# Kernel tuning notes

Measured on AMD Instinct MI355X. Metric: run time of the kernel, lower is better.

## Reference

```python
import jax, jax.numpy as jnp
import numpy as np

HIDDEN_DIM = 32
EDGE_DIM = 16
EDGE_HIDDEN = 64
N_EDGES = 250000


def setup_inputs() -> dict:
    key = jax.random.key(0)
    k1, k2, k3, k4, k5 = jax.random.split(key, 5)
    h_v = jax.random.normal(k1, (N_EDGES, HIDDEN_DIM), dtype=jnp.float32)
    h_w = jax.random.normal(k2, (N_EDGES, HIDDEN_DIM), dtype=jnp.float32)
    edge_features = jax.random.normal(k3, (N_EDGES, EDGE_DIM), dtype=jnp.float32)
    # Edge-network MLP params: edge_dim -> edge_hidden -> hidden_dim^2
    W1 = jax.random.normal(k4, (EDGE_DIM, EDGE_HIDDEN), dtype=jnp.float32) * (1.0 / np.sqrt(EDGE_DIM))
    b1 = jnp.zeros((EDGE_HIDDEN,), dtype=jnp.float32)
    W2 = jax.random.normal(k5, (EDGE_HIDDEN, HIDDEN_DIM * HIDDEN_DIM), dtype=jnp.float32) * (1.0 / np.sqrt(EDGE_HIDDEN))
    b2 = jnp.zeros((HIDDEN_DIM * HIDDEN_DIM,), dtype=jnp.float32)
    return {"h_v": h_v, "h_w": h_w, "edge_features": edge_features,
            "W1": W1, "b1": b1, "W2": W2, "b2": b2}


def reference(h_v, h_w, edge_features, W1, b1, W2, b2):
    # 1. Edge MLP: (n_edges, edge_dim) -> (n_edges, d*d)
    hdn = jax.nn.relu(edge_features @ W1 + b1)          # (E, edge_hidden)
    A = (hdn @ W2 + b2)                                  # (E, d*d)
    # 2. Reshape to per-edge matrices (E, d, d)
    d = h_w.shape[-1]
    A = A.reshape(-1, d, d)
    # 3. Per-edge matrix-vector product: M = A(e_vw) @ h_w
    messages = jnp.einsum('eij,ej->ei', A, h_w)          # (E, d)
    return messages
```

## Files before the change

### kernel.cpp

```cpp
#include <hip/hip_runtime.h>

typedef unsigned short u16;
typedef _Float16 f16x2 __attribute__((ext_vector_type(2)));
typedef _Float16 f16x8 __attribute__((ext_vector_type(8)));
typedef float    f32x4  __attribute__((ext_vector_type(4)));
typedef float    f32x16 __attribute__((ext_vector_type(16)));


union U4 { uint4 u; f16x8 h; u16 s[8]; };
union HU { f16x2 h2[4]; f16x8 h8; };

__global__ void prep_kernel(const float* __restrict__ W1,
                            const float* __restrict__ W2,
                            const float* __restrict__ b2,
                            u16* __restrict__ ws)
{
    int id = blockIdx.x * 256 + threadIdx.x;
    if (id < 8320) {
        int k2 = id >> 6, l = id & 63;
        int h = l >> 5, col = l & 31;
        U4 o;
        #pragma unroll
        for (int g = 0; g < 2; ++g) {
            int base4 = k2 * 16 + g * 8 + h * 4;
            f32x4 v;
            if (base4 < 2048) {
                int k1 = base4 >> 5, j32 = base4 & 31;
                v = *(const f32x4*)&W2[k1 * 1024 + col * 32 + j32];
            } else {
                v = *(const f32x4*)&b2[col * 32 + (base4 - 2048)];
            }
            #pragma unroll
            for (int j = 0; j < 4; ++j)
                o.h[g * 4 + j] = (_Float16)v[j];
        }
        *(uint4*)(ws + id * 8) = o.u;
    } else if (id < 8448) {
        int idx = id - 8320;
        int nt = idx >> 6, l = idx & 63;
        int h = l >> 5, col = nt * 32 + (l & 31);
        U4 o;
        #pragma unroll
        for (int g = 0; g < 2; ++g)
            #pragma unroll
            for (int j = 0; j < 4; ++j) {
                int k = g * 8 + h * 4 + j;
                o.h[g * 4 + j] = (_Float16)W1[k * 64 + col];
            }
        *(uint4*)(ws + id * 8) = o.u;
    }
}

#define STRIDE_T 98
#define SLICE_T  6400

__global__ __launch_bounds__(256, 3) void edge_kernel(
    const float* __restrict__ h_w,
    const float* __restrict__ ef,
    const float* __restrict__ b1,
    const u16*  __restrict__ ws,
    float* __restrict__ out,
    int E)
{
    __shared__ alignas(16) u16 ldsT[4 * SLICE_T];
    const int tid  = threadIdx.x;
    const int lane = tid & 63;
    const int wv   = tid >> 6;
    const int l31  = lane & 31;
    const int h    = lane >> 5;
    const int tileBase = (blockIdx.x * 4 + wv) * 96;
    if (tileBase >= E) return;
    u16* myT = ldsT + wv * SLICE_T;

    const uint4* Bf  = (const uint4*)ws;
    const uint4* W1f = (const uint4*)(ws + 8320 * 8);

    U4 w0, w1;
    w0.u = W1f[lane];
    w1.u = W1f[64 + lane];
    const float bb0 = b1[l31], bb1 = b1[32 + l31];
    #pragma unroll
    for (int mt = 0; mt < 3; ++mt) {
        int e = tileBase + mt * 32 + l31;
        bool ok = e < E;
        f32x4 g0 = {}, g1 = {};
        if (ok) {
            g0 = *(const f32x4*)&ef[e * 16 + h * 4];
            g1 = *(const f32x4*)&ef[e * 16 + 8 + h * 4];
        }
        U4 a;
        #pragma unroll
        for (int j = 0; j < 4; ++j) {
            a.h[j]     = (_Float16)g0[j];
            a.h[4 + j] = (_Float16)g1[j];
        }
        f32x16 c0 = {}, c1 = {};
        c0 = __builtin_amdgcn_mfma_f32_32x32x16_f16(a.h, w0.h, c0, 0, 0, 0);
        c1 = __builtin_amdgcn_mfma_f32_32x32x16_f16(a.h, w1.h, c1, 0, 0, 0);
        #pragma unroll
        for (int nt = 0; nt < 2; ++nt) {
            float bb = nt ? bb1 : bb0;
            int k1 = nt * 32 + l31;
            #pragma unroll
            for (int rp = 0; rp < 8; ++rp) {
                int r = 2 * rp;
                float v0 = fmaxf((nt ? c1[r]     : c0[r])     + bb, 0.f);
                float v1 = fmaxf((nt ? c1[r + 1] : c0[r + 1]) + bb, 0.f);
                f16x2 p = { (_Float16)v0, (_Float16)v1 };
                int e0 = mt * 32 + (r & 3) + 8 * (r >> 2) + 4 * h;
                *(unsigned int*)(myT + k1 * STRIDE_T + e0) =
                    __builtin_bit_cast(unsigned int, p);
            }
        }
    }
    if (lane < 48)
        *(unsigned int*)(myT + 64 * STRIDE_T + lane * 2) = 0x3C003C00u;

    f16x2 hwA[3][2][4];
    #pragma unroll
    for (int mt = 0; mt < 3; ++mt) {
        int e = tileBase + mt * 32 + l31;
        bool ok = e < E;
        f32x4 q0 = {}, q1 = {}, q2 = {}, q3 = {};
        if (ok) {
            const float* hp = h_w + (size_t)e * 32 + h * 4;
            q0 = *(const f32x4*)(hp);
            q1 = *(const f32x4*)(hp + 8);
            q2 = *(const f32x4*)(hp + 16);
            q3 = *(const f32x4*)(hp + 24);
        }
        hwA[mt][0][0] = f16x2{ (_Float16)q0[0], (_Float16)q0[1] };
        hwA[mt][0][1] = f16x2{ (_Float16)q0[2], (_Float16)q0[3] };
        hwA[mt][0][2] = f16x2{ (_Float16)q1[0], (_Float16)q1[1] };
        hwA[mt][0][3] = f16x2{ (_Float16)q1[2], (_Float16)q1[3] };
        hwA[mt][1][0] = f16x2{ (_Float16)q2[0], (_Float16)q2[1] };
        hwA[mt][1][1] = f16x2{ (_Float16)q2[2], (_Float16)q2[3] };
        hwA[mt][1][2] = f16x2{ (_Float16)q3[0], (_Float16)q3[1] };
        hwA[mt][1][3] = f16x2{ (_Float16)q3[2], (_Float16)q3[3] };
    }

    f32x16 acc0 = {}, acc1 = {}, acc2 = {};

    const uint4* bp = Bf + lane;
    #pragma unroll 2
    for (int k1 = 0; k1 < 65; ++k1) {
        U4 bf0, bf1;
        bf0.u = bp[(2 * k1) * 64];
        bf1.u = bp[(2 * k1 + 1) * 64];
        u16 t0 = myT[k1 * STRIDE_T + l31];
        u16 t1 = myT[k1 * STRIDE_T + 32 + l31];
        u16 t2 = myT[k1 * STRIDE_T + 64 + l31];
        #pragma unroll
        for (int mt = 0; mt < 3; ++mt) {
            union { u16 u; _Float16 f; } cv;
            cv.u = (mt == 0) ? t0 : (mt == 1) ? t1 : t2;
            f16x2 hh = { cv.f, cv.f };
            HU A;
            #pragma unroll
            for (int rr = 0; rr < 4; ++rr) A.h2[rr] = hh * hwA[mt][0][rr];
            if (mt == 0)      acc0 = __builtin_amdgcn_mfma_f32_32x32x16_f16(A.h8, bf0.h, acc0, 0, 0, 0);
            else if (mt == 1) acc1 = __builtin_amdgcn_mfma_f32_32x32x16_f16(A.h8, bf0.h, acc1, 0, 0, 0);
            else              acc2 = __builtin_amdgcn_mfma_f32_32x32x16_f16(A.h8, bf0.h, acc2, 0, 0, 0);
            #pragma unroll
            for (int rr = 0; rr < 4; ++rr) A.h2[rr] = hh * hwA[mt][1][rr];
            if (mt == 0)      acc0 = __builtin_amdgcn_mfma_f32_32x32x16_f16(A.h8, bf1.h, acc0, 0, 0, 0);
            else if (mt == 1) acc1 = __builtin_amdgcn_mfma_f32_32x32x16_f16(A.h8, bf1.h, acc1, 0, 0, 0);
            else              acc2 = __builtin_amdgcn_mfma_f32_32x32x16_f16(A.h8, bf1.h, acc2, 0, 0, 0);
        }
    }

    #pragma unroll
    for (int mt = 0; mt < 3; ++mt) {
        #pragma unroll
        for (int r = 0; r < 16; ++r) {
            int row = (r & 3) + 8 * (r >> 2) + 4 * h;
            int e = tileBase + mt * 32 + row;
            float v = (mt == 0) ? acc0[r] : (mt == 1) ? acc1[r] : acc2[r];
            if (e < E) out[(size_t)e * 32 + l31] = v;
        }
    }
}

extern "C" void kernel_launch(void* const* d_in, const int* in_sizes, int n_in,
                              void* d_out, int out_size, void* d_ws, size_t ws_size,
                              hipStream_t stream)
{
    const float* h_w = (const float*)d_in[1];
    const float* ef  = (const float*)d_in[2];
    const float* W1  = (const float*)d_in[3];
    const float* b1  = (const float*)d_in[4];
    const float* W2  = (const float*)d_in[5];
    const float* b2  = (const float*)d_in[6];
    float* out = (float*)d_out;
    const int E = in_sizes[1] / 32;
    u16* ws = (u16*)d_ws;

    prep_kernel<<<33, 256, 0, stream>>>(W1, W2, b2, ws);

    const int blocks = (E + 4 * 96 - 1) / (4 * 96);
    edge_kernel<<<blocks, 256, 0, stream>>>(h_w, ef, b1, ws, out, E);
}
```

Measured before the change: 49.19 us.

## Shrink per-wave tile to 64 edges and software-pipeline weight loads

Each wave now processes 64 edges instead of 96, which shrinks the LDS slice and the accumulator registers so the occupancy hint can rise from 3 to 4 blocks per CU. The global loads of the combined W2/b2 fragments are prefetched into a 4-deep register ring ahead of the MFMA loop, and the LDS hidden-activation values are loaded one iteration ahead. This is meant to hide global and LDS latency behind the matrix ops. In exchange, every wave re-reads the same weight stream for fewer edges, so total weight traffic per edge goes up.

```diff
diff --git a/kernel.cpp b/kernel.cpp
--- a/kernel.cpp
+++ b/kernel.cpp
@@ -51,10 +51,10 @@
     }
 }
 
-#define STRIDE_T 98
-#define SLICE_T  6400
-
-__global__ __launch_bounds__(256, 3) void edge_kernel(
+#define STRIDE_T 66
+#define SLICE_T  4352
+
+__global__ __launch_bounds__(256, 4) void edge_kernel(
     const float* __restrict__ h_w,
     const float* __restrict__ ef,
     const float* __restrict__ b1,
@@ -68,19 +68,27 @@
     const int wv   = tid >> 6;
     const int l31  = lane & 31;
     const int h    = lane >> 5;
-    const int tileBase = (blockIdx.x * 4 + wv) * 96;
+    const int tileBase = (blockIdx.x * 4 + wv) * 64;
     if (tileBase >= E) return;
     u16* myT = ldsT + wv * SLICE_T;
 
     const uint4* Bf  = (const uint4*)ws;
     const uint4* W1f = (const uint4*)(ws + 8320 * 8);
+    const uint4* bp  = Bf + lane;
+
+    U4 pipe[4][2];
+    #pragma unroll
+    for (int p = 0; p < 4; ++p) {
+        pipe[p][0].u = bp[(2 * p) * 64];
+        pipe[p][1].u = bp[(2 * p + 1) * 64];
+    }
 
     U4 w0, w1;
     w0.u = W1f[lane];
     w1.u = W1f[64 + lane];
     const float bb0 = b1[l31], bb1 = b1[32 + l31];
     #pragma unroll
-    for (int mt = 0; mt < 3; ++mt) {
+    for (int mt = 0; mt < 2; ++mt) {
         int e = tileBase + mt * 32 + l31;
         bool ok = e < E;
         f32x4 g0 = {}, g1 = {};
@@ -113,12 +121,12 @@
             }
         }
     }
-    if (lane < 48)
+    if (lane < 32)
         *(unsigned int*)(myT + 64 * STRIDE_T + lane * 2) = 0x3C003C00u;
 
-    f16x2 hwA[3][2][4];
-    #pragma unroll
-    for (int mt = 0; mt < 3; ++mt) {
+    f16x2 hwA[2][2][4];
+    #pragma unroll
+    for (int mt = 0; mt < 2; ++mt) {
         int e = tileBase + mt * 32 + l31;
         bool ok = e < E;
         f32x4 q0 = {}, q1 = {}, q2 = {}, q3 = {};
@@ -139,43 +147,48 @@
         hwA[mt][1][3] = f16x2{ (_Float16)q3[2], (_Float16)q3[3] };
     }
 
-    f32x16 acc0 = {}, acc1 = {}, acc2 = {};
-
-    const uint4* bp = Bf + lane;
-    #pragma unroll 2
+    f32x16 acc0 = {}, acc1 = {};
+
+    u16 t0 = myT[l31];
+    u16 t1 = myT[32 + l31];
+    #pragma unroll 4
     for (int k1 = 0; k1 < 65; ++k1) {
-        U4 bf0, bf1;
-        bf0.u = bp[(2 * k1) * 64];
-        bf1.u = bp[(2 * k1 + 1) * 64];
-        u16 t0 = myT[k1 * STRIDE_T + l31];
-        u16 t1 = myT[k1 * STRIDE_T + 32 + l31];
-        u16 t2 = myT[k1 * STRIDE_T + 64 + l31];
-        #pragma unroll
-        for (int mt = 0; mt < 3; ++mt) {
+        const int slot = k1 & 3;
+        const u16 c0v = t0, c1v = t1;
+        {
+            int kn = (k1 + 1 <= 64) ? k1 + 1 : 64;
+            t0 = myT[kn * STRIDE_T + l31];
+            t1 = myT[kn * STRIDE_T + 32 + l31];
+        }
+        #pragma unroll
+        for (int mt = 0; mt < 2; ++mt) {
             union { u16 u; _Float16 f; } cv;
-            cv.u = (mt == 0) ? t0 : (mt == 1) ? t1 : t2;
+            cv.u = (mt == 0) ? c0v : c1v;
             f16x2 hh = { cv.f, cv.f };
             HU A;
             #pragma unroll
             for (int rr = 0; rr < 4; ++rr) A.h2[rr] = hh * hwA[mt][0][rr];
-            if (mt == 0)      acc0 = __builtin_amdgcn_mfma_f32_32x32x16_f16(A.h8, bf0.h, acc0, 0, 0, 0);
-            else if (mt == 1) acc1 = __builtin_amdgcn_mfma_f32_32x32x16_f16(A.h8, bf0.h, acc1, 0, 0, 0);
-            else              acc2 = __builtin_amdgcn_mfma_f32_32x32x16_f16(A.h8, bf0.h, acc2, 0, 0, 0);
+            if (mt == 0) acc0 = __builtin_amdgcn_mfma_f32_32x32x16_f16(A.h8, pipe[slot][0].h, acc0, 0, 0, 0);
+            else         acc1 = __builtin_amdgcn_mfma_f32_32x32x16_f16(A.h8, pipe[slot][0].h, acc1, 0, 0, 0);
             #pragma unroll
             for (int rr = 0; rr < 4; ++rr) A.h2[rr] = hh * hwA[mt][1][rr];
-            if (mt == 0)      acc0 = __builtin_amdgcn_mfma_f32_32x32x16_f16(A.h8, bf1.h, acc0, 0, 0, 0);
-            else if (mt == 1) acc1 = __builtin_amdgcn_mfma_f32_32x32x16_f16(A.h8, bf1.h, acc1, 0, 0, 0);
-            else              acc2 = __builtin_amdgcn_mfma_f32_32x32x16_f16(A.h8, bf1.h, acc2, 0, 0, 0);
-        }
-    }
-
-    #pragma unroll
-    for (int mt = 0; mt < 3; ++mt) {
+            if (mt == 0) acc0 = __builtin_amdgcn_mfma_f32_32x32x16_f16(A.h8, pipe[slot][1].h, acc0, 0, 0, 0);
+            else         acc1 = __builtin_amdgcn_mfma_f32_32x32x16_f16(A.h8, pipe[slot][1].h, acc1, 0, 0, 0);
+        }
+        {
+            int kp = (k1 + 4 <= 64) ? k1 + 4 : 64;
+            pipe[slot][0].u = bp[(2 * kp) * 64];
+            pipe[slot][1].u = bp[(2 * kp + 1) * 64];
+        }
+    }
+
+    #pragma unroll
+    for (int mt = 0; mt < 2; ++mt) {
         #pragma unroll
         for (int r = 0; r < 16; ++r) {
             int row = (r & 3) + 8 * (r >> 2) + 4 * h;
             int e = tileBase + mt * 32 + row;
-            float v = (mt == 0) ? acc0[r] : (mt == 1) ? acc1[r] : acc2[r];
+            float v = (mt == 0) ? acc0[r] : acc1[r];
             if (e < E) out[(size_t)e * 32 + l31] = v;
         }
     }
@@ -197,6 +210,6 @@
 
     prep_kernel<<<33, 256, 0, stream>>>(W1, W2, b2, ws);
 
-    const int blocks = (E + 4 * 96 - 1) / (4 * 96);
+    const int blocks = (E + 4 * 64 - 1) / (4 * 64);
     edge_kernel<<<blocks, 256, 0, stream>>>(h_w, ef, b1, ws, out, E);
 }
```

After: 47.29 us. 3.9% less time.
